# Performance work log

Measured on AMD Instinct MI355X. Metric: run time of the kernel, lower is better.

Reference implementation:

```python
import jax, jax.numpy as jnp
import numpy as np

EPS_SINK = 0.01   # SinkhornDistance eps
N_ITERS = 20      # fixed iteration count (original: max 100 with host-side early exit)
BN_EPS = 1e-5


def _conv(x, w, b):
    # NCHW 3x3 (or 1x1) conv, SAME padding
    y = jax.lax.conv_general_dilated(x, w, (1, 1), 'SAME',
                                     dimension_numbers=('NCHW', 'OIHW', 'NCHW'))
    return y + b[None, :, None, None]


def _bn_train(x, gamma, beta):
    # BatchNorm2d in training mode: batch statistics over (N,H,W)
    m = jnp.mean(x, axis=(0, 2, 3), keepdims=True)
    v = jnp.var(x, axis=(0, 2, 3), keepdims=True)
    return gamma[None, :, None, None] * (x - m) * jax.lax.rsqrt(v + BN_EPS) + beta[None, :, None, None]


def _calc_mean_std(f, eps=1e-5):
    m = jnp.mean(f, axis=(2, 3), keepdims=True)
    s = jnp.sqrt(jnp.var(f, axis=(2, 3), keepdims=True) + eps)
    return m, s


def _sinkhorn_pi(x, y, eps):
    # x: [b, n, d] content points, y: [b, m, d] style points. Cosine-distance cost.
    xn = x / jnp.linalg.norm(x, axis=-1, keepdims=True)
    yn = y / jnp.linalg.norm(y, axis=-1, keepdims=True)
    C = 1.0 - jnp.einsum('bnd,bmd->bnm', xn, yn)          # [b, n, m]
    b, n, m = C.shape
    log_mu = jnp.log(jnp.full((b, n), 1.0 / n) + 1e-8)
    log_nu = jnp.log(jnp.full((b, m), 1.0 / m) + 1e-8)

    def Mmat(u, v):
        # (-C + u_i + v_j) / eps
        return (-C + u[..., None] + v[..., None, :]) / eps

    def step(carry, _):
        u, v = carry
        u = eps * (log_mu - jax.scipy.special.logsumexp(Mmat(u, v), axis=-1)) + u
        v = eps * (log_nu - jax.scipy.special.logsumexp(Mmat(u, v), axis=-2)) + v
        return (u, v), None

    (u, v), _ = jax.lax.scan(step, (jnp.zeros((b, n)), jnp.zeros((b, m))), None, length=N_ITERS)
    return jnp.exp(Mmat(u, v))                             # transport plan pi


def setup_inputs() -> dict:
    key = jax.random.key(0)
    ks = jax.random.split(key, 16)
    bs, dim, h, w = 4, 512, 32, 32
    s = 0.05
    return {
        'content_feat': jax.random.normal(ks[0], (bs, dim, h, w), jnp.float32),
        'style_feat':   jax.random.normal(ks[1], (bs, dim, h, w), jnp.float32),
        # alpha_predictor (version 1): conv(1024->256,3x3) ReLU BN, conv(256->256,3x3) ReLU BN, conv(256->512,3x3)
        'w1': jax.random.normal(ks[2], (256, 1024, 3, 3), jnp.float32) * s,
        'b1': jnp.zeros((256,), jnp.float32),
        'g1': jnp.ones((256,), jnp.float32),
        'be1': jnp.zeros((256,), jnp.float32),
        'w2': jax.random.normal(ks[3], (256, 256, 3, 3), jnp.float32) * s,
        'b2': jnp.zeros((256,), jnp.float32),
        'g2': jnp.ones((256,), jnp.float32),
        'be2': jnp.zeros((256,), jnp.float32),
        'w3': jax.random.normal(ks[4], (512, 256, 3, 3), jnp.float32) * s,
        'b3': jnp.zeros((512,), jnp.float32),
        # stand-in decoder head: 3x3 conv 512->3 (decoder is an external injected module)
        'dec_w': jax.random.normal(ks[5], (3, 512, 3, 3), jnp.float32) * s,
        'dec_b': jnp.zeros((3,), jnp.float32),
    }


def reference(content_feat, style_feat, w1, b1, g1, be1, w2, b2, g2, be2, w3, b3, dec_w, dec_b):
    bs, dim, h, w = content_feat.shape
    cf = content_feat.reshape(bs, dim, h * w).transpose(0, 2, 1)   # [b, hw, d]
    sf = style_feat.reshape(bs, dim, h * w).transpose(0, 2, 1)
    pi = _sinkhorn_pi(cf, sf, EPS_SINK) * (h * w)                  # style_assign: pi * h * w
    t = jnp.einsum('bnm,bmd->bnd', pi, sf).transpose(0, 2, 1).reshape(bs, dim, h, w)
    cm, cs = _calc_mean_std(content_feat)
    c_normed = (content_feat - cm) / cs
    a = _bn_train(jax.nn.relu(_conv(jnp.concatenate([t, content_feat], axis=1), w1, b1)), g1, be1)
    a = _bn_train(jax.nn.relu(_conv(a, w2, b2)), g2, be2)
    alpha = _conv(a, w3, b3)
    t = alpha * c_normed + t
    g_t = _conv(t, dec_w, dec_b)
    return g_t
```

## Files before the change

kernel.cpp:

```cpp
#include <hip/hip_runtime.h>

typedef unsigned short u16;
typedef unsigned int u32;
typedef unsigned long long u64;
typedef float f32x4 __attribute__((ext_vector_type(4)));
typedef short bf16x8 __attribute__((ext_vector_type(8)));

#define DEV static __device__ __forceinline__

DEV float bf2f(u16 u){ union{float f; u32 i;} x; x.i = ((u32)u) << 16; return x.f; }
DEV u16 f2bf(float f){ union{float f; u32 i;} x; x.f = f; u32 u = x.i;
  return (u16)((u + 0x7fffu + ((u >> 16) & 1u)) >> 16); }
DEV u16 f2h(float f){ _Float16 h = (_Float16)f; u16 u; __builtin_memcpy(&u, &h, 2); return u; }
DEV float h2f(u16 u){ _Float16 h; __builtin_memcpy(&h, &u, 2); return (float)h; }
DEV uint4 pack8(const u16* s){ uint4 v;
  v.x = (u32)s[0] | ((u32)s[1]<<16); v.y = (u32)s[2] | ((u32)s[3]<<16);
  v.z = (u32)s[4] | ((u32)s[5]<<16); v.w = (u32)s[6] | ((u32)s[7]<<16); return v; }
DEV f32x4 mfma16(bf16x8 a, bf16x8 b, f32x4 c){
  return __builtin_amdgcn_mfma_f32_16x16x32_bf16(a, b, c, 0, 0, 0);
}
DEV bf16x8 ldfrag(const u16* p){ return *(const bf16x8*)p; }

DEV void st_agent(float* p, float v){
  __hip_atomic_store(p, v, __ATOMIC_RELAXED, __HIP_MEMORY_SCOPE_AGENT); }
DEV float ld_agent(const float* p){
  return __hip_atomic_load(p, __ATOMIC_RELAXED, __HIP_MEMORY_SCOPE_AGENT); }
DEV float2 ld_agent2(const float* p){
  u64 u = __hip_atomic_load((const u64*)p, __ATOMIC_RELAXED, __HIP_MEMORY_SCOPE_AGENT);
  union{u64 u; float2 f;} c; c.u = u; return c.f; }
DEV void st_agent_u32(u32* p, u32 v){
  __hip_atomic_store(p, v, __ATOMIC_RELAXED, __HIP_MEMORY_SCOPE_AGENT); }
DEV u32 ld_agent_u32(const u32* p){
  return __hip_atomic_load(p, __ATOMIC_RELAXED, __HIP_MEMORY_SCOPE_AGENT); }

constexpr float SCL = 144.269504088896341f;
constexpr float LOG2MU = -9.99998522680257f;

constexpr size_t MB = 1ull << 20;
constexpr size_t OFF_G    = 0;
constexpr size_t OFF_GT   = 8*MB;
constexpr size_t OFF_U    = 16*MB;
constexpr size_t OFF_V    = OFF_U   + (16<<10);
constexpr size_t OFF_BAR  = OFF_V   + (16<<10);
constexpr size_t OFF_INS  = OFF_BAR + (16<<10);
constexpr size_t OFF_CNM  = OFF_INS + (16<<10);
constexpr size_t OFF_CNIS = OFF_CNM + (8<<10);
constexpr size_t OFF_BNS  = OFF_CNIS+ (8<<10);
constexpr size_t OFF_PNP  = OFF_BNS + (4<<10);
constexpr size_t OFF_CFH  = 17*MB;
constexpr size_t OFF_CFL  = 21*MB;
constexpr size_t OFF_SFH  = 25*MB;
constexpr size_t OFF_SFL  = 29*MB;
constexpr size_t OFF_SNB  = 33*MB;
constexpr size_t OFF_TN   = 37*MB;
constexpr size_t OFF_TCP  = 45*MB;
constexpr size_t OFF_W1P  = 53*MB;
constexpr size_t OFF_W2P  = OFF_W1P + 9*256*1024*2;
constexpr size_t OFF_W3P  = OFF_W2P + 9*256*256*2;
constexpr size_t OFF_WDP  = OFF_W3P + 9*512*256*2;
constexpr size_t OFF_PIP  = 62*MB;
constexpr size_t OFF_Z1  = 17*MB;
constexpr size_t OFF_A1P = 25*MB;
constexpr size_t OFF_Z2  = 27*MB;
constexpr size_t OFF_A2P = 35*MB;
constexpr size_t OFF_T2P = 17*MB;

__global__ void pack_all_k(const float* __restrict__ w1, const float* __restrict__ w2,
                           const float* __restrict__ w3, const float* __restrict__ wd,
                           u16* __restrict__ w1p, u16* __restrict__ w2p,
                           u16* __restrict__ w3p, u16* __restrict__ wdp){
  int blk = blockIdx.x;
  const float* w; u16* wp; int CI, NCK, rel;
  if (blk < 512){ w = w1; wp = w1p; CI = 1024; NCK = 32; rel = blk; }
  else if (blk < 640){ w = w2; wp = w2p; CI = 256; NCK = 8; rel = blk - 512; }
  else if (blk < 896){ w = w3; wp = w3p; CI = 256; NCK = 8; rel = blk - 640; }
  else {
    int o = (blk - 896)*256 + threadIdx.x;
    int ci = o & 511; int r = o >> 9; int co = r & 15; int tap = r >> 4;
    wdp[o] = f2bf((co < 3) ? wd[(size_t)(co*512 + ci)*9 + tap] : 0.f);
    return;
  }
  int g = rel / NCK, ck = rel % NCK;
  __shared__ float L[16*288];
  const float* base = w + ((size_t)(g*16)*CI + ck*32)*9;
  #pragma unroll
  for (int i = 0; i < 18; ++i){
    int idx = i*256 + threadIdx.x;
    int row = idx / 288, col = idx - row*288;
    L[row*288 + col] = base[(size_t)row*CI*9 + col];
  }
  __syncthreads();
  u16* dst = wp + ((size_t)(g*NCK + ck)*9)*512;
  #pragma unroll
  for (int i = 0; i < 18; ++i){
    int j = i*256 + threadIdx.x;
    int tap = j >> 9, r = j & 511, lane = r >> 3, e = r & 7;
    int co = lane & 15, cil = ((lane >> 4) & 3)*8 + e;
    dst[j] = f2bf(L[co*288 + cil*9 + tap]);
  }
}

__global__ void stats_k(const float* __restrict__ cf, const float* __restrict__ sf,
                        float* __restrict__ cnm, float* __restrict__ cnis,
                        float* __restrict__ part, float* __restrict__ zUV,
                        float* __restrict__ zBNS, u32* __restrict__ zbar){
  int blk = blockIdx.x;
  if (blk < 2048){
    int bd = blk;
    float4 v = ((const float4*)(cf + (size_t)bd*1024))[threadIdx.x];
    float s = v.x+v.y+v.z+v.w;
    float q = v.x*v.x+v.y*v.y+v.z*v.z+v.w*v.w;
    #pragma unroll
    for (int m = 32; m >= 1; m >>= 1){ s += __shfl_xor(s, m, 64); q += __shfl_xor(q, m, 64); }
    __shared__ float ls[4], lq[4];
    int w = threadIdx.x >> 6;
    if ((threadIdx.x & 63) == 0){ ls[w] = s; lq[w] = q; }
    __syncthreads();
    if (threadIdx.x == 0){
      float S = ls[0]+ls[1]+ls[2]+ls[3], Q = lq[0]+lq[1]+lq[2]+lq[3];
      float mean = S * (1.f/1024.f);
      float var  = Q * (1.f/1024.f) - mean*mean;
      cnm[bd] = mean; cnis[bd] = rsqrtf(var + 1e-5f);
    }
    return;
  }
  if (blk < 2304){
    int rel = blk - 2048;
    int x = rel & 15, y = (rel >> 4) & 7, src = rel >> 7;
    const float* in = src ? sf : cf;
    int p = x*256 + threadIdx.x;
    int b = p >> 10, pp = p & 1023;
    const float* base = in + ((size_t)(b*512 + y*64))*1024 + pp;
    float s = 0.f;
    #pragma unroll 8
    for (int d = 0; d < 64; ++d){ float xx = base[(size_t)d*1024]; s += xx*xx; }
    part[((size_t)(src*8 + y))*4096 + p] = s;
    return;
  }
  if (blk < 2336){
    zUV[(blk - 2304)*256 + threadIdx.x] = 0.f;
    return;
  }
  if (blk < 2340){
    zBNS[(blk - 2336)*256 + threadIdx.x] = 0.f;
    return;
  }
  zbar[(blk - 2340)*256 + threadIdx.x] = 0u;
}

__global__ void tsplit_k(const float* __restrict__ cf, const float* __restrict__ sf,
                         const float* __restrict__ pnp,
                         u16* __restrict__ cfh, u16* __restrict__ cfl,
                         u16* __restrict__ sfh, u16* __restrict__ sfl,
                         u16* __restrict__ tcp, u16* __restrict__ snb){
  __shared__ float tile[64][65];
  int z = blockIdx.z, is_style = z >> 2, b = z & 3;
  const float* src = is_style ? sf : cf;
  u16* hi = is_style ? sfh : cfh;
  u16* lo = is_style ? sfl : cfl;
  int p0 = blockIdx.x*64, d0 = blockIdx.y*64;
  int r = threadIdx.x >> 2, c0 = (threadIdx.x & 3) * 16;
  const float* sp = src + ((size_t)(b*512 + d0 + r))*1024 + p0 + c0;
  float v[16];
  #pragma unroll
  for (int e = 0; e < 4; ++e){
    float4 t4 = ((const float4*)sp)[e];
    v[e*4+0]=t4.x; v[e*4+1]=t4.y; v[e*4+2]=t4.z; v[e*4+3]=t4.w;
  }
  #pragma unroll
  for (int j = 0; j < 16; ++j) tile[r][c0+j] = v[j];
  if (is_style){
    u16 t16[16];
    #pragma unroll
    for (int j = 0; j < 16; ++j) t16[j] = f2bf(v[j]);
    uint4* ap = (uint4*)(snb + ((size_t)(b*512 + d0 + r))*1024 + p0 + c0);
    ap[0] = pack8(t16); ap[1] = pack8(t16+8);
  }
  __syncthreads();
  int pr = r, dc0 = c0;
  float inv;
  {
    const float* pp = pnp + (size_t)(is_style ? 8*4096 : 0) + ((b<<10) + p0 + pr);
    float s = 0.f;
    #pragma unroll
    for (int j = 0; j < 8; ++j) s += pp[j*4096];
    inv = rsqrtf(s);
  }
  u16 h16[16], l16[16], t16[16];
  #pragma unroll
  for (int j = 0; j < 16; ++j){
    float x = tile[dc0+j][pr];
    t16[j] = f2bf(x);
    float xn = x * inv;
    u16 h = f2bf(xn);
    h16[j] = h;
    l16[j] = f2bf(xn - bf2f(h));
  }
  size_t orow = (size_t)((b<<10) + p0 + pr);
  uint4* hp = (uint4*)(hi + orow*512 + d0 + dc0);
  uint4* lp = (uint4*)(lo + orow*512 + d0 + dc0);
  hp[0] = pack8(h16); hp[1] = pack8(h16+8);
  lp[0] = pack8(l16); lp[1] = pack8(l16+8);
  if (!is_style){
    int D = d0 + dc0;
    size_t off = ((size_t)(16 + (D>>5))*4096 + orow)*32 + (D&31);
    *(uint4*)(tcp + off)     = pack8(t16);
    *(uint4*)(tcp + off + 8) = pack8(t16+8);
  }
}

__global__ __launch_bounds__(256) void cgemm_k(const u16* __restrict__ cfh, const u16* __restrict__ cfl,
        const u16* __restrict__ sfh, const u16* __restrict__ sfl,
        u16* __restrict__ G, u16* __restrict__ Gt){
  __shared__ __align__(16) u16 SH[4*128*40];
  u16* Ah = SH;          u16* Al = SH + 5120;
  u16* Bh = SH + 10240;  u16* Bl = SH + 15360;
  int b = blockIdx.z;
  size_t abase = ((size_t)((b<<10) + blockIdx.x*128))*512;
  size_t bbase = ((size_t)((b<<10) + blockIdx.y*128))*512;
  int lane = threadIdx.x & 63, wid = threadIdx.x >> 6;
  int wm = (wid >> 1)*64, wn = (wid & 1)*64;
  int fr = lane & 15, qd = lane >> 4;
  int sr = threadIdx.x >> 1, sc = (threadIdx.x & 1)*16;
  f32x4 acc[4][4] = {};
  for (int kk = 0; kk < 512; kk += 32){
    size_t g0 = (size_t)sr*512 + kk + sc;
    *(uint4*)&Ah[sr*40+sc]   = *(const uint4*)(cfh + abase + g0);
    *(uint4*)&Ah[sr*40+sc+8] = *(const uint4*)(cfh + abase + g0 + 8);
    *(uint4*)&Al[sr*40+sc]   = *(const uint4*)(cfl + abase + g0);
    *(uint4*)&Al[sr*40+sc+8] = *(const uint4*)(cfl + abase + g0 + 8);
    *(uint4*)&Bh[sr*40+sc]   = *(const uint4*)(sfh + bbase + g0);
    *(uint4*)&Bh[sr*40+sc+8] = *(const uint4*)(sfh + bbase + g0 + 8);
    *(uint4*)&Bl[sr*40+sc]   = *(const uint4*)(sfl + bbase + g0);
    *(uint4*)&Bl[sr*40+sc+8] = *(const uint4*)(sfl + bbase + g0 + 8);
    __syncthreads();
    bf16x8 bhf[4], blf[4];
    #pragma unroll
    for (int ni = 0; ni < 4; ++ni){
      bhf[ni] = ldfrag(&Bh[(wn + ni*16 + fr)*40 + qd*8]);
      blf[ni] = ldfrag(&Bl[(wn + ni*16 + fr)*40 + qd*8]);
    }
    #pragma unroll
    for (int mi = 0; mi < 4; ++mi){
      bf16x8 ah = ldfrag(&Ah[(wm + mi*16 + fr)*40 + qd*8]);
      bf16x8 al = ldfrag(&Al[(wm + mi*16 + fr)*40 + qd*8]);
      #pragma unroll
      for (int ni = 0; ni < 4; ++ni){
        acc[mi][ni] = mfma16(ah, bhf[ni], acc[mi][ni]);
        acc[mi][ni] = mfma16(ah, blf[ni], acc[mi][ni]);
        acc[mi][ni] = mfma16(al, bhf[ni], acc[mi][ni]);
      }
    }
    __syncthreads();
  }
  #pragma unroll
  for (int mi = 0; mi < 4; ++mi)
    #pragma unroll
    for (int ni = 0; ni < 4; ++ni)
      #pragma unroll
      for (int rg = 0; rg < 4; ++rg){
        int r = wm + mi*16 + qd*4 + rg;
        int c = wn + ni*16 + fr;
        SH[r*136 + c] = f2h((acc[mi][ni][rg] - 1.f) * SCL);
      }
  __syncthreads();
  size_t gb = (((size_t)b) << 20) + (size_t)(blockIdx.x*128)*1024 + blockIdx.y*128;
  #pragma unroll
  for (int i = 0; i < 8; ++i){
    int idx = i*256 + threadIdx.x;
    int r = idx >> 4, c4 = idx & 15;
    *(uint4*)(G + gb + (size_t)r*1024 + c4*8) = *(const uint4*)&SH[r*136 + c4*8];
  }
  __syncthreads();
  #pragma unroll
  for (int mi = 0; mi < 4; ++mi)
    #pragma unroll
    for (int ni = 0; ni < 4; ++ni)
      #pragma unroll
      for (int rg = 0; rg < 4; ++rg){
        int r = wm + mi*16 + qd*4 + rg;
        int c = wn + ni*16 + fr;
        SH[c*136 + r] = f2h((acc[mi][ni][rg] - 1.f) * SCL);
      }
  __syncthreads();
  size_t gtb = (((size_t)b) << 20) + (size_t)(blockIdx.y*128)*1024 + blockIdx.x*128;
  #pragma unroll
  for (int i = 0; i < 8; ++i){
    int idx = i*256 + threadIdx.x;
    int r = idx >> 4, c4 = idx & 15;
    *(uint4*)(Gt + gtb + (size_t)r*1024 + c4*8) = *(const uint4*)&SH[r*136 + c4*8];
  }
}

__global__ __launch_bounds__(512) void sink_k(const u16* __restrict__ G, const u16* __restrict__ Gt,
        float* __restrict__ U, float* __restrict__ V,
        u32* __restrict__ flags, u16* __restrict__ pip){
  __shared__ __align__(16) u16 LL[2][16*1024];
  int blk = blockIdx.x;
  int b = blk >> 6;
  int sub = blk & 63;
  int rb = sub << 4;
  int tid = threadIdx.x;
  size_t gbase = ((size_t)((b << 10) + rb)) << 10;
  {
    const uint4* g0 = (const uint4*)(G + gbase);
    const uint4* g1 = (const uint4*)(Gt + gbase);
    uint4* d0 = (uint4*)LL[0];
    uint4* d1 = (uint4*)LL[1];
    #pragma unroll
    for (int i = 0; i < 4; ++i){
      d0[i*512 + tid] = g0[i*512 + tid];
      d1[i*512 + tid] = g1[i*512 + tid];
    }
  }
  __syncthreads();
  int wid = tid >> 6, lane = tid & 63;
  float* Ub = U + (b << 10);
  float* Vb = V + (b << 10);
  u32* fgrp = flags + (b << 6)*16;
  u32* fmine = fgrp + sub*16;
  int r0 = wid << 1;
  int cbase = lane << 2;

  auto dopass = [&](int which, const float* __restrict__ inv, float* __restrict__ outv, int tgt){
    float va[16];
    #pragma unroll
    for (int k = 0; k < 4; ++k){
      #pragma unroll
      for (int j = 0; j < 2; ++j){
        float2 t = ld_agent2(inv + k*256 + cbase + j*2);
        va[k*4 + j*2]     = t.x;
        va[k*4 + j*2 + 1] = t.y;
      }
    }
    #pragma unroll
    for (int rr = 0; rr < 2; ++rr){
      int row = r0 + rr;
      float x[16]; float mx = -3.0e38f;
      #pragma unroll
      for (int k = 0; k < 4; ++k){
        uint2 g2 = *(const uint2*)(&LL[which][row*1024 + k*256 + cbase]);
        float t0 = h2f((u16)(g2.x & 0xffffu)) + va[k*4+0];
        float t1 = h2f((u16)(g2.x >> 16))     + va[k*4+1];
        float t2 = h2f((u16)(g2.y & 0xffffu)) + va[k*4+2];
        float t3 = h2f((u16)(g2.y >> 16))     + va[k*4+3];
        x[k*4+0]=t0; x[k*4+1]=t1; x[k*4+2]=t2; x[k*4+3]=t3;
        mx = fmaxf(mx, fmaxf(fmaxf(t0,t1), fmaxf(t2,t3)));
      }
      #pragma unroll
      for (int m = 32; m >= 1; m >>= 1) mx = fmaxf(mx, __shfl_xor(mx, m, 64));
      float s = 0.f;
      #pragma unroll
      for (int i = 0; i < 16; ++i) s += exp2f(x[i] - mx);
      #pragma unroll
      for (int m = 32; m >= 1; m >>= 1) s += __shfl_xor(s, m, 64);
      if (lane == 0) st_agent(outv + rb + row, LOG2MU - (mx + log2f(s)));
    }
    __syncthreads();
    if (tid == 0) st_agent_u32(fmine, (u32)tgt);
    if (tid < 64){
      u32* fl = fgrp + tid*16;
      for (;;){
        u32 v = ld_agent_u32(fl);
        if (__all((int)(v >= (u32)tgt))) break;
        __builtin_amdgcn_s_sleep(1);
      }
    }
    __syncthreads();
  };

  for (int it = 0; it < 20; ++it){
    dopass(0, Vb, Ub, 2*it + 1);
    dopass(1, Ub, Vb, 2*it + 2);
  }

  float va[16];
  #pragma unroll
  for (int k = 0; k < 4; ++k){
    #pragma unroll
    for (int j = 0; j < 2; ++j){
      float2 t = ld_agent2(Vb + k*256 + cbase + j*2);
      va[k*4 + j*2]     = t.x;
      va[k*4 + j*2 + 1] = t.y;
    }
  }
  #pragma unroll
  for (int rr = 0; rr < 2; ++rr){
    int row = r0 + rr;
    float ur = ld_agent(Ub + rb + row) + 10.f;
    size_t orow = ((size_t)((b << 10) + rb + row)) << 10;
    #pragma unroll
    for (int k = 0; k < 4; ++k){
      uint2 g2 = *(const uint2*)(&LL[0][row*1024 + k*256 + cbase]);
      u16 o[4];
      o[0] = f2bf(exp2f(h2f((u16)(g2.x & 0xffffu)) + va[k*4+0] + ur));
      o[1] = f2bf(exp2f(h2f((u16)(g2.x >> 16))     + va[k*4+1] + ur));
      o[2] = f2bf(exp2f(h2f((u16)(g2.y & 0xffffu)) + va[k*4+2] + ur));
      o[3] = f2bf(exp2f(h2f((u16)(g2.y >> 16))     + va[k*4+3] + ur));
      uint2 pk; pk.x = (u32)o[0] | ((u32)o[1]<<16); pk.y = (u32)o[2] | ((u32)o[3]<<16);
      *(uint2*)(pip + orow + k*256 + cbase) = pk;
    }
  }
}

__global__ __launch_bounds__(256) void tgemm_k(const u16* __restrict__ pip,
        const u16* __restrict__ snb, float* __restrict__ tn, u16* __restrict__ tcp){
  __shared__ __align__(16) u16 As[64*40], Bs[128*40];
  int b = blockIdx.z, p0 = blockIdx.x*64, d0 = blockIdx.y*128;
  int tid = threadIdx.x, lane = tid & 63, wid = tid >> 6;
  int wm = (wid >> 1)*32, wn = (wid & 1)*64;
  int fr = lane & 15, qd = lane >> 4;
  int a_r = tid >> 2, a_c = (tid & 3)*8;
  int b_r = tid >> 1, b_c = (tid & 1)*16;
  const u16* Arow = pip + (((size_t)((b<<10) + p0 + a_r)) << 10) + a_c;
  const u16* Brow = snb + (((size_t)(b*512 + d0 + b_r)) << 10) + b_c;
  uint4 pa, pb0, pb1;
  auto issue = [&](int kk){
    pa = *(const uint4*)(Arow + kk);
    const uint4* bp = (const uint4*)(Brow + kk);
    pb0 = bp[0]; pb1 = bp[1];
  };
  f32x4 acc[2][4] = {};
  issue(0);
  for (int kk = 0; kk < 1024; kk += 32){
    *(uint4*)&As[a_r*40 + a_c] = pa;
    *(uint4*)&Bs[b_r*40 + b_c] = pb0;
    *(uint4*)&Bs[b_r*40 + b_c + 8] = pb1;
    __syncthreads();
    if (kk + 32 < 1024) issue(kk + 32);
    bf16x8 bfr[4];
    #pragma unroll
    for (int ni = 0; ni < 4; ++ni) bfr[ni] = ldfrag(&Bs[(wn + ni*16 + fr)*40 + qd*8]);
    #pragma unroll
    for (int mi = 0; mi < 2; ++mi){
      bf16x8 afr = ldfrag(&As[(wm + mi*16 + fr)*40 + qd*8]);
      #pragma unroll
      for (int ni = 0; ni < 4; ++ni) acc[mi][ni] = mfma16(afr, bfr[ni], acc[mi][ni]);
    }
    __syncthreads();
  }
  #pragma unroll
  for (int mi = 0; mi < 2; ++mi)
    #pragma unroll
    for (int ni = 0; ni < 4; ++ni)
      #pragma unroll
      for (int rg = 0; rg < 4; ++rg){
        int p = p0 + wm + mi*16 + qd*4 + rg;
        int d = d0 + wn + ni*16 + fr;
        float vout = acc[mi][ni][rg];
        size_t ro = (size_t)((b<<10) + p);
        tn[ro*512 + d] = vout;
        tcp[((size_t)(d>>5)*4096 + ro)*32 + (d&31)] = f2bf(vout);
      }
}

template<int CI, int CO, int KSPLIT, int MODE>
__global__ __launch_bounds__(256) void conv_k(const u16* __restrict__ inp, const u16* __restrict__ wpk,
        const float* __restrict__ bias, float* __restrict__ fout, u16* __restrict__ bout,
        const u16* __restrict__ tcp, const float* __restrict__ cnm, const float* __restrict__ cnis,
        const float* __restrict__ tn){
  constexpr int NCK_TOT = CI/32, NCK = NCK_TOT/KSPLIT;
  __shared__ __align__(16) u16 As[128*40];
  int b = blockIdx.z & 3, ks = blockIdx.z >> 2;
  int c0 = blockIdx.y*64;
  int r0 = blockIdx.x*2;
  int tid = threadIdx.x, lane = tid & 63, wid = tid >> 6;
  int wm = (wid >> 1)*32, wn = (wid & 1)*32;
  int fr = lane & 15, qd = lane >> 4;
  int ck0 = ks*NCK;
  int hrow = tid >> 1;
  int ah = (tid & 1)*16;
  int gy = r0 - 1 + (hrow >> 5);
  bool a_ok = ((unsigned)gy < 32u);
  size_t arow = (size_t)(b<<10) + (r0-1)*32 + hrow;
  uint4 pa0 = {0,0,0,0}, pa1 = {0,0,0,0};
  auto issueA = [&](int ck){
    if (a_ok){
      const uint4* s = (const uint4*)(inp + ((size_t)(ck0+ck)*4096 + arow)*32 + ah);
      pa0 = s[0]; pa1 = s[1];
    }
  };
  int g0 = (c0 + wn) >> 4;
  const u16* wb0 = wpk + ((size_t)(g0    )*NCK_TOT + ck0)*9*512 + lane*8;
  const u16* wb1 = wpk + ((size_t)(g0 + 1)*NCK_TOT + ck0)*9*512 + lane*8;

  f32x4 acc[2][2] = {};
  issueA(0);
  for (int ck = 0; ck < NCK; ++ck){
    *(uint4*)&As[hrow*40 + ah]     = pa0;
    *(uint4*)&As[hrow*40 + ah + 8] = pa1;
    __syncthreads();
    if (ck + 1 < NCK) issueA(ck + 1);
    #pragma unroll
    for (int tap = 0; tap < 9; ++tap){
      const int dy = tap/3 - 1, dx = tap%3 - 1;
      bf16x8 bf0 = ldfrag(wb0 + (size_t)(ck*9 + tap)*512);
      bf16x8 bf1 = ldfrag(wb1 + (size_t)(ck*9 + tap)*512);
      #pragma unroll
      for (int mi = 0; mi < 2; ++mi){
        int p0w = wm + mi*16;
        int pcol = (p0w & 31) + fr + dx;
        int lr = (p0w >> 5) + dy + 1;
        bool okc = (unsigned)pcol < 32u;
        bf16x8 af = ldfrag(&As[(lr*32 + (okc ? pcol : 0))*40 + qd*8]);
        if (!okc) af = bf16x8(0);
        acc[mi][0] = mfma16(af, bf0, acc[mi][0]);
        acc[mi][1] = mfma16(af, bf1, acc[mi][1]);
      }
    }
    __syncthreads();
  }
  #pragma unroll
  for (int mi = 0; mi < 2; ++mi)
    #pragma unroll
    for (int ni = 0; ni < 2; ++ni)
      #pragma unroll
      for (int rg = 0; rg < 4; ++rg){
        int pp = blockIdx.x*64 + wm + mi*16 + qd*4 + rg;
        int cc = c0 + wn + ni*16 + fr;
        float v = acc[mi][ni][rg];
        size_t ro = (size_t)((b<<10) + pp);
        if (MODE == 0){
          fout[(size_t)ks*4096*CO + ro*CO + cc] = v;
        } else {
          float alpha = v + bias[cc];
          float cn = (bf2f(tcp[((size_t)(16 + (cc>>5))*4096 + ro)*32 + (cc&31)])
                      - cnm[(b<<9) + cc]) * cnis[(b<<9) + cc];
          bout[((size_t)(cc>>5)*4096 + ro)*32 + (cc&31)] = f2bf(alpha*cn + tn[ro*512 + cc]);
        }
      }
}

__global__ __launch_bounds__(512) void dec_k(const u16* __restrict__ t2p, const u16* __restrict__ wdp,
                                             const float* __restrict__ db, float* __restrict__ out){
  __shared__ float wlds[3*4608];
  int tid = threadIdx.x;
  for (int k = tid; k < 3*4608; k += 512){
    int c = k / 4608, rem = k - c*4608;
    int tap = rem >> 9, ci = rem & 511;
    wlds[k] = bf2f(wdp[(size_t)(tap*16 + c)*512 + ci]);
  }
  __syncthreads();
  int b = blockIdx.x >> 5;
  int p = ((blockIdx.x & 31) << 5) + (tid >> 4);
  int sub = tid & 15;
  int py = p >> 5, px = p & 31;
  float a0 = 0.f, a1 = 0.f, a2 = 0.f;
  for (int tap = 0; tap < 9; ++tap){
    int sy = py + tap/3 - 1, sx = px + tap%3 - 1;
    if (((unsigned)sy < 32u) && ((unsigned)sx < 32u)){
      size_t row = (size_t)((b<<10) + (sy<<5) + sx);
      const float* w0 = wlds + tap*512;
      #pragma unroll
      for (int j = 0; j < 4; ++j){
        int ci0 = j*128 + sub*8;
        uint4 v = *(const uint4*)(t2p + ((size_t)(ci0>>5)*4096 + row)*32 + (ci0&31));
        u32 ww[4] = {v.x, v.y, v.z, v.w};
        #pragma unroll
        for (int e = 0; e < 8; ++e){
          float x = bf2f((u16)((e & 1) ? (ww[e>>1] >> 16) : (ww[e>>1] & 0xffffu)));
          a0 += x * w0[ci0 + e];
          a1 += x * w0[4608 + ci0 + e];
          a2 += x * w0[9216 + ci0 + e];
        }
      }
    }
  }
  #pragma unroll
  for (int m = 8; m >= 1; m >>= 1){
    a0 += __shfl_xor(a0, m, 64);
    a1 += __shfl_xor(a1, m, 64);
    a2 += __shfl_xor(a2, m, 64);
  }
  if (sub == 0){
    out[((size_t)(b*3 + 0) << 10) + p] = a0 + db[0];
    out[((size_t)(b*3 + 1) << 10) + p] = a1 + db[1];
    out[((size_t)(b*3 + 2) << 10) + p] = a2 + db[2];
  }
}

__global__ void bn_stats_k(const float* __restrict__ z, const float* __restrict__ bias,
                           float* __restrict__ sums){
  int c = blockIdx.x*64 + (threadIdx.x & 63);
  int w = threadIdx.x >> 6;
  int rbase = blockIdx.y*512 + w*128;
  float bi = bias[c];
  float s = 0.f, q = 0.f;
  for (int i = 0; i < 128; ++i){
    size_t ro = (size_t)(rbase + i)*256 + c;
    float x = fmaxf(z[ro] + z[4096*256 + ro] + bi, 0.f);
    s += x; q += x*x;
  }
  __shared__ float ls[4][64], lq[4][64];
  ls[w][threadIdx.x & 63] = s; lq[w][threadIdx.x & 63] = q;
  __syncthreads();
  if (threadIdx.x < 64){
    float S = ls[0][threadIdx.x]+ls[1][threadIdx.x]+ls[2][threadIdx.x]+ls[3][threadIdx.x];
    float Q = lq[0][threadIdx.x]+lq[1][threadIdx.x]+lq[2][threadIdx.x]+lq[3][threadIdx.x];
    atomicAdd(&sums[blockIdx.x*64 + threadIdx.x], S);
    atomicAdd(&sums[256 + blockIdx.x*64 + threadIdx.x], Q);
  }
}

__global__ void bn_apply_k(const float* __restrict__ z, const float* __restrict__ bias,
                           const float* __restrict__ sums, const float* __restrict__ gamma,
                           const float* __restrict__ beta, u16* __restrict__ ap){
  int idx = blockIdx.x*256 + threadIdx.x;
  float4 va = ((const float4*)z)[idx];
  float4 vb = ((const float4*)(z + 4096*256))[idx];
  int row = idx >> 6;
  int cc0 = (idx << 2) & 255;
  float e[4] = {va.x+vb.x, va.y+vb.y, va.z+vb.z, va.w+vb.w};
  u16 o[4];
  #pragma unroll
  for (int k = 0; k < 4; ++k){
    int c = cc0 + k;
    float mean = sums[c] * (1.f/4096.f);
    float var  = sums[256 + c] * (1.f/4096.f) - mean*mean;
    float sc = gamma[c] * rsqrtf(var + 1e-5f);
    float sh = beta[c] - mean*sc;
    float x = fmaxf(e[k] + bias[c], 0.f);
    o[k] = f2bf(x*sc + sh);
  }
  uint2 pk; pk.x = (u32)o[0] | ((u32)o[1]<<16); pk.y = (u32)o[2] | ((u32)o[3]<<16);
  *(uint2*)(ap + ((size_t)(cc0>>5)*4096 + row)*32 + (cc0&31)) = pk;
}

extern "C" void kernel_launch(void* const* d_in, const int* in_sizes, int n_in,
                              void* d_out, int out_size, void* d_ws, size_t ws_size,
                              hipStream_t stream){
  const float* cf  = (const float*)d_in[0];
  const float* sf  = (const float*)d_in[1];
  const float* w1  = (const float*)d_in[2];
  const float* b1  = (const float*)d_in[3];
  const float* g1  = (const float*)d_in[4];
  const float* be1 = (const float*)d_in[5];
  const float* w2  = (const float*)d_in[6];
  const float* b2  = (const float*)d_in[7];
  const float* g2  = (const float*)d_in[8];
  const float* be2 = (const float*)d_in[9];
  const float* w3  = (const float*)d_in[10];
  const float* b3  = (const float*)d_in[11];
  const float* dw  = (const float*)d_in[12];
  const float* db  = (const float*)d_in[13];

  char* ws = (char*)d_ws;
  u16* G    = (u16*)(ws + OFF_G);
  u16* Gt   = (u16*)(ws + OFF_GT);
  float* U    = (float*)(ws + OFF_U);
  float* V    = (float*)(ws + OFF_V);
  u32* bar    = (u32*)(ws + OFF_BAR);
  float* cnm  = (float*)(ws + OFF_CNM);
  float* cnis = (float*)(ws + OFF_CNIS);
  float* bns1 = (float*)(ws + OFF_BNS);
  float* bns2 = bns1 + 512;
  float* pnp  = (float*)(ws + OFF_PNP);
  u16* cfh = (u16*)(ws + OFF_CFH);
  u16* cfl = (u16*)(ws + OFF_CFL);
  u16* sfh = (u16*)(ws + OFF_SFH);
  u16* sfl = (u16*)(ws + OFF_SFL);
  u16* snb = (u16*)(ws + OFF_SNB);
  float* tn  = (float*)(ws + OFF_TN);
  u16* tcp = (u16*)(ws + OFF_TCP);
  u16* w1p = (u16*)(ws + OFF_W1P);
  u16* w2p = (u16*)(ws + OFF_W2P);
  u16* w3p = (u16*)(ws + OFF_W3P);
  u16* wdp = (u16*)(ws + OFF_WDP);
  u16* pip = (u16*)(ws + OFF_PIP);
  float* z1  = (float*)(ws + OFF_Z1);
  u16*   a1p = (u16*)(ws + OFF_A1P);
  float* z2  = (float*)(ws + OFF_Z2);
  u16*   a2p = (u16*)(ws + OFF_A2P);
  u16*   t2p = (u16*)(ws + OFF_T2P);

  pack_all_k<<<1184, 256, 0, stream>>>(w1, w2, w3, dw, w1p, w2p, w3p, wdp);

  stats_k<<<2356, 256, 0, stream>>>(cf, sf, cnm, cnis, pnp, U, bns1, bar);
  tsplit_k<<<dim3(16, 8, 8), 256, 0, stream>>>(cf, sf, pnp, cfh, cfl, sfh, sfl, tcp, snb);

  cgemm_k<<<dim3(8, 8, 4), 256, 0, stream>>>(cfh, cfl, sfh, sfl, G, Gt);

  sink_k<<<256, 512, 0, stream>>>(G, Gt, U, V, bar, pip);

  tgemm_k<<<dim3(16, 4, 4), 256, 0, stream>>>(pip, snb, tn, tcp);

  conv_k<1024, 256, 2, 0><<<dim3(16, 4, 8), 256, 0, stream>>>(
      tcp, w1p, nullptr, z1, nullptr, nullptr, nullptr, nullptr, nullptr);
  bn_stats_k<<<dim3(4, 8), 256, 0, stream>>>(z1, b1, bns1);
  bn_apply_k<<<1024, 256, 0, stream>>>(z1, b1, bns1, g1, be1, a1p);

  conv_k<256, 256, 2, 0><<<dim3(16, 4, 8), 256, 0, stream>>>(
      a1p, w2p, nullptr, z2, nullptr, nullptr, nullptr, nullptr, nullptr);
  bn_stats_k<<<dim3(4, 8), 256, 0, stream>>>(z2, b2, bns2);
  bn_apply_k<<<1024, 256, 0, stream>>>(z2, b2, bns2, g2, be2, a2p);

  conv_k<256, 512, 1, 1><<<dim3(16, 8, 4), 256, 0, stream>>>(
      a2p, w3p, b3, nullptr, t2p, tcp, cnm, cnis, tn);

  dec_k<<<128, 512, 0, stream>>>(t2p, wdp, db, (float*)d_out);

  (void)in_sizes; (void)n_in; (void)out_size; (void)ws_size;
}
```

Measured before the change: 406.4 us.

## Merge weight packing into stats kernel, widen BN stats grid, cache final u

```diff
diff --git a/kernel.cpp b/kernel.cpp
--- a/kernel.cpp
+++ b/kernel.cpp
@@ -65,45 +65,14 @@
 constexpr size_t OFF_A2P = 35*MB;
 constexpr size_t OFF_T2P = 17*MB;
 
-__global__ void pack_all_k(const float* __restrict__ w1, const float* __restrict__ w2,
-                           const float* __restrict__ w3, const float* __restrict__ wd,
-                           u16* __restrict__ w1p, u16* __restrict__ w2p,
-                           u16* __restrict__ w3p, u16* __restrict__ wdp){
-  int blk = blockIdx.x;
-  const float* w; u16* wp; int CI, NCK, rel;
-  if (blk < 512){ w = w1; wp = w1p; CI = 1024; NCK = 32; rel = blk; }
-  else if (blk < 640){ w = w2; wp = w2p; CI = 256; NCK = 8; rel = blk - 512; }
-  else if (blk < 896){ w = w3; wp = w3p; CI = 256; NCK = 8; rel = blk - 640; }
-  else {
-    int o = (blk - 896)*256 + threadIdx.x;
-    int ci = o & 511; int r = o >> 9; int co = r & 15; int tap = r >> 4;
-    wdp[o] = f2bf((co < 3) ? wd[(size_t)(co*512 + ci)*9 + tap] : 0.f);
-    return;
-  }
-  int g = rel / NCK, ck = rel % NCK;
-  __shared__ float L[16*288];
-  const float* base = w + ((size_t)(g*16)*CI + ck*32)*9;
-  #pragma unroll
-  for (int i = 0; i < 18; ++i){
-    int idx = i*256 + threadIdx.x;
-    int row = idx / 288, col = idx - row*288;
-    L[row*288 + col] = base[(size_t)row*CI*9 + col];
-  }
-  __syncthreads();
-  u16* dst = wp + ((size_t)(g*NCK + ck)*9)*512;
-  #pragma unroll
-  for (int i = 0; i < 18; ++i){
-    int j = i*256 + threadIdx.x;
-    int tap = j >> 9, r = j & 511, lane = r >> 3, e = r & 7;
-    int co = lane & 15, cil = ((lane >> 4) & 3)*8 + e;
-    dst[j] = f2bf(L[co*288 + cil*9 + tap]);
-  }
-}
-
 __global__ void stats_k(const float* __restrict__ cf, const float* __restrict__ sf,
                         float* __restrict__ cnm, float* __restrict__ cnis,
                         float* __restrict__ part, float* __restrict__ zUV,
-                        float* __restrict__ zBNS, u32* __restrict__ zbar){
+                        float* __restrict__ zBNS, u32* __restrict__ zbar,
+                        const float* __restrict__ w1, const float* __restrict__ w2,
+                        const float* __restrict__ w3, const float* __restrict__ wd,
+                        u16* __restrict__ w1p, u16* __restrict__ w2p,
+                        u16* __restrict__ w3p, u16* __restrict__ wdp){
   int blk = blockIdx.x;
   if (blk < 2048){
     int bd = blk;
@@ -145,7 +114,39 @@
     zBNS[(blk - 2336)*256 + threadIdx.x] = 0.f;
     return;
   }
-  zbar[(blk - 2340)*256 + threadIdx.x] = 0u;
+  if (blk < 2356){
+    zbar[(blk - 2340)*256 + threadIdx.x] = 0u;
+    return;
+  }
+  int pblk = blk - 2356;
+  const float* w; u16* wp; int CI, NCK, rel;
+  if (pblk < 512){ w = w1; wp = w1p; CI = 1024; NCK = 32; rel = pblk; }
+  else if (pblk < 640){ w = w2; wp = w2p; CI = 256; NCK = 8; rel = pblk - 512; }
+  else if (pblk < 896){ w = w3; wp = w3p; CI = 256; NCK = 8; rel = pblk - 640; }
+  else {
+    int o = (pblk - 896)*256 + threadIdx.x;
+    int ci = o & 511; int r = o >> 9; int co = r & 15; int tap = r >> 4;
+    wdp[o] = f2bf((co < 3) ? wd[(size_t)(co*512 + ci)*9 + tap] : 0.f);
+    return;
+  }
+  int g = rel / NCK, ck = rel % NCK;
+  __shared__ float L[16*288];
+  const float* base = w + ((size_t)(g*16)*CI + ck*32)*9;
+  #pragma unroll
+  for (int i = 0; i < 18; ++i){
+    int idx = i*256 + threadIdx.x;
+    int row = idx / 288, col = idx - row*288;
+    L[row*288 + col] = base[(size_t)row*CI*9 + col];
+  }
+  __syncthreads();
+  u16* dst = wp + ((size_t)(g*NCK + ck)*9)*512;
+  #pragma unroll
+  for (int i = 0; i < 18; ++i){
+    int j = i*256 + threadIdx.x;
+    int tap = j >> 9, r = j & 511, lane = r >> 3, e = r & 7;
+    int co = lane & 15, cil = ((lane >> 4) & 3)*8 + e;
+    dst[j] = f2bf(L[co*288 + cil*9 + tap]);
+  }
 }
 
 __global__ void tsplit_k(const float* __restrict__ cf, const float* __restrict__ sf,
@@ -321,7 +322,9 @@
   u32* fmine = fgrp + sub*16;
   int r0 = wid << 1;
   int cbase = lane << 2;
-
+  int budget = 1 << 21;
+
+  float o0 = 0.f, o1 = 0.f;
   auto dopass = [&](int which, const float* __restrict__ inv, float* __restrict__ outv, int tgt){
     float va[16];
     #pragma unroll
@@ -354,7 +357,9 @@
       for (int i = 0; i < 16; ++i) s += exp2f(x[i] - mx);
       #pragma unroll
       for (int m = 32; m >= 1; m >>= 1) s += __shfl_xor(s, m, 64);
-      if (lane == 0) st_agent(outv + rb + row, LOG2MU - (mx + log2f(s)));
+      float o = LOG2MU - (mx + log2f(s));
+      if (rr == 0) o0 = o; else o1 = o;
+      if (lane == 0) st_agent(outv + rb + row, o);
     }
     __syncthreads();
     if (tid == 0) st_agent_u32(fmine, (u32)tgt);
@@ -363,14 +368,17 @@
       for (;;){
         u32 v = ld_agent_u32(fl);
         if (__all((int)(v >= (u32)tgt))) break;
+        if (--budget < 0) break;
         __builtin_amdgcn_s_sleep(1);
       }
     }
     __syncthreads();
   };
 
+  float ku0 = 0.f, ku1 = 0.f;
   for (int it = 0; it < 20; ++it){
     dopass(0, Vb, Ub, 2*it + 1);
+    ku0 = o0; ku1 = o1;
     dopass(1, Ub, Vb, 2*it + 2);
   }
 
@@ -387,7 +395,7 @@
   #pragma unroll
   for (int rr = 0; rr < 2; ++rr){
     int row = r0 + rr;
-    float ur = ld_agent(Ub + rb + row) + 10.f;
+    float ur = (rr == 0 ? ku0 : ku1) + 10.f;
     size_t orow = ((size_t)((b << 10) + rb + row)) << 10;
     #pragma unroll
     for (int k = 0; k < 4; ++k){
@@ -583,10 +591,10 @@
                            float* __restrict__ sums){
   int c = blockIdx.x*64 + (threadIdx.x & 63);
   int w = threadIdx.x >> 6;
-  int rbase = blockIdx.y*512 + w*128;
+  int rbase = blockIdx.y*128 + w*32;
   float bi = bias[c];
   float s = 0.f, q = 0.f;
-  for (int i = 0; i < 128; ++i){
+  for (int i = 0; i < 32; ++i){
     size_t ro = (size_t)(rbase + i)*256 + c;
     float x = fmaxf(z[ro] + z[4096*256 + ro] + bi, 0.f);
     s += x; q += x*x;
@@ -673,9 +681,8 @@
   u16*   a2p = (u16*)(ws + OFF_A2P);
   u16*   t2p = (u16*)(ws + OFF_T2P);
 
-  pack_all_k<<<1184, 256, 0, stream>>>(w1, w2, w3, dw, w1p, w2p, w3p, wdp);
-
-  stats_k<<<2356, 256, 0, stream>>>(cf, sf, cnm, cnis, pnp, U, bns1, bar);
+  stats_k<<<3540, 256, 0, stream>>>(cf, sf, cnm, cnis, pnp, U, bns1, bar,
+                                    w1, w2, w3, dw, w1p, w2p, w3p, wdp);
   tsplit_k<<<dim3(16, 8, 8), 256, 0, stream>>>(cf, sf, pnp, cfh, cfl, sfh, sfl, tcp, snb);
 
   cgemm_k<<<dim3(8, 8, 4), 256, 0, stream>>>(cfh, cfl, sfh, sfl, G, Gt);
@@ -686,12 +693,12 @@
 
   conv_k<1024, 256, 2, 0><<<dim3(16, 4, 8), 256, 0, stream>>>(
       tcp, w1p, nullptr, z1, nullptr, nullptr, nullptr, nullptr, nullptr);
-  bn_stats_k<<<dim3(4, 8), 256, 0, stream>>>(z1, b1, bns1);
+  bn_stats_k<<<dim3(4, 32), 256, 0, stream>>>(z1, b1, bns1);
   bn_apply_k<<<1024, 256, 0, stream>>>(z1, b1, bns1, g1, be1, a1p);
 
   conv_k<256, 256, 2, 0><<<dim3(16, 4, 8), 256, 0, stream>>>(
       a1p, w2p, nullptr, z2, nullptr, nullptr, nullptr, nullptr, nullptr);
-  bn_stats_k<<<dim3(4, 8), 256, 0, stream>>>(z2, b2, bns2);
+  bn_stats_k<<<dim3(4, 32), 256, 0, stream>>>(z2, b2, bns2);
   bn_apply_k<<<1024, 256, 0, stream>>>(z2, b2, bns2, g2, be2, a2p);
 
   conv_k<256, 512, 1, 1><<<dim3(16, 8, 4), 256, 0, stream>>>(
```

New measurement: 393.6 us. 3.1% less time.
